# Optimization experiments

Measured on AMD Instinct MI355X. Metric: run time of the kernel, lower is better.

## Reference

```python
import jax, jax.numpy as jnp
import numpy as np

THRE = 4.0  # ReLUX threshold / multispike lens
EPS = 1e-5  # BatchNorm eps (torch default)

@jax.custom_vjp
def spike(x):
    # multispike forward: floor(clamp(x,0,4)+0.5)
    return jnp.floor(jnp.clip(x, 0.0, THRE) + 0.5)

def _spike_fwd(x):
    return spike(x), x

def _spike_bwd(x, g):
    # surrogate gradient: pass-through on 0 < x < lens
    return (g * ((x > 0) & (x < THRE)).astype(g.dtype),)

spike.defvjp(_spike_fwd, _spike_bwd)


def setup_inputs() -> dict:
    key = jax.random.key(0)
    k0, k1, k2 = jax.random.split(key, 3)
    B, N, C = 4, 1024, 512
    x = jax.random.normal(k0, (B, N, C), jnp.float32)
    Wqkv = jax.random.normal(k1, (3 * C, C), jnp.float32) * (C ** -0.5)  # Linear weight [out,in], no bias
    gamma = jnp.ones((3 * C,), jnp.float32)   # BN weight
    beta = jnp.zeros((3 * C,), jnp.float32)   # BN bias
    Wproj = jax.random.normal(k2, (C, C), jnp.float32) * (C ** -0.5)
    bproj = jnp.zeros((C,), jnp.float32)
    return {"x": x, "Wqkv": Wqkv, "gamma": gamma, "beta": beta, "Wproj": Wproj, "bproj": bproj}


def reference(x, Wqkv, gamma, beta, Wproj, bproj):
    B, N, C = x.shape
    H = 8
    hd = C // H
    scale = hd ** -0.5

    xs = spike(x)                                    # head_spike
    qkv = jnp.einsum('bnc,dc->bnd', xs, Wqkv)        # [B,N,3C]
    # BatchNorm1d over channel dim with batch stats across (B, N)
    mu = qkv.mean(axis=(0, 1))
    var = qkv.var(axis=(0, 1))
    qkv = (qkv - mu) * jax.lax.rsqrt(var + EPS) * gamma + beta

    qkv = qkv.reshape(B, N, 3, H, hd).transpose(2, 0, 3, 1, 4)  # [3,B,H,N,hd]
    q = spike(qkv[0])
    k = spike(qkv[1])
    v = spike(qkv[2])

    attn = jnp.einsum('bhnd,bhmd->bhnm', q, k)       # no softmax
    attn = spike(attn)
    out = jnp.einsum('bhnm,bhmd->bhnd', attn, v) * scale
    out = out.transpose(0, 2, 1, 3).reshape(B, N, C)
    out = spike(out)                                 # project_spike
    return jnp.einsum('bnc,dc->bnd', out, Wproj) + bproj
```

## Files before the change

### kernel.cpp

```cpp
#include <hip/hip_runtime.h>

typedef __attribute__((ext_vector_type(8))) short short8;
typedef __attribute__((ext_vector_type(4))) float f32x4;
typedef __attribute__((ext_vector_type(4))) int int4v;
typedef __attribute__((ext_vector_type(4))) unsigned int u32x4;

#define THRE 4.0f

#define GLOAD_LDS16(g, l) \
    __builtin_amdgcn_global_load_lds((const __attribute__((address_space(1))) void*)(g), \
                                     (__attribute__((address_space(3))) void*)(l), 16, 0, 0)

__device__ __forceinline__ float spikef(float x) {
    return floorf(fminf(fmaxf(x, 0.0f), THRE) + 0.5f);
}
__device__ __forceinline__ unsigned short f2bf(float f) {
    return (unsigned short)(__builtin_bit_cast(unsigned int, f) >> 16);
}
__device__ __forceinline__ unsigned short f2bf_rn(float f) {
    unsigned u = __builtin_bit_cast(unsigned int, f);
    unsigned r = ((u >> 16) & 1u) + 0x7FFFu;
    return (unsigned short)((u + r) >> 16);
}
__device__ __forceinline__ float bf2f(unsigned short s) {
    return __builtin_bit_cast(float, (unsigned int)s << 16);
}
__device__ __forceinline__ int4v mfma_i8(u32x4 a, u32x4 b, int4v c) {
    return __builtin_amdgcn_mfma_i32_16x16x64_i8(__builtin_bit_cast(int4v, a),
                                                 __builtin_bit_cast(int4v, b), c, 0, 0, 0);
}

__global__ void k_prep(const float* __restrict__ x,
                       const float* __restrict__ Wq, const float* __restrict__ Wp,
                       short* __restrict__ xs, short* __restrict__ Wqd, short* __restrict__ Wpd) {
    int i = blockIdx.x * 256 + threadIdx.x;
    if (i < 2097152) {
        xs[i] = (short)f2bf(spikef(x[i]));
    } else if (i < 2883584) {
        int j = i - 2097152;
        Wqd[j] = (short)(__builtin_bit_cast(unsigned int, Wq[j]) >> 16);
    } else {
        int j = i - 2883584;
        Wpd[j] = (short)(__builtin_bit_cast(unsigned int, Wp[j]) >> 16);
    }
}

__global__ __launch_bounds__(256) void k_gemm_qkv(const short* __restrict__ A,
                                                  const short* __restrict__ B,
                                                  short* __restrict__ C,
                                                  float* __restrict__ psum,
                                                  float* __restrict__ psq) {
    __shared__ __align__(16) short As[128 * 64];
    __shared__ __align__(16) short Bs[96 * 64];
    const int tid  = threadIdx.x;
    const int lane = tid & 63, wv = tid >> 6;
    const int wy = wv >> 1, wx = wv & 1;
    const int quad = lane >> 4, l16 = lane & 15;
    const int m0 = blockIdx.y * 128, n0 = blockIdx.x * 96;
    const int K = 512, N = 1536;

    f32x4 acc[4][3];
    #pragma unroll
    for (int i = 0; i < 4; ++i)
        #pragma unroll
        for (int j = 0; j < 3; ++j)
            #pragma unroll
            for (int r = 0; r < 4; ++r) acc[i][j][r] = 0.f;

    const short* gA[4]; short* lA[4];
    #pragma unroll
    for (int i = 0; i < 4; ++i) {
        int L = wv + 4 * i;
        int c = L * 64 + lane;
        int r = c >> 3, g = (c & 7) ^ (r & 7);
        gA[i] = A + (size_t)(m0 + r) * K + g * 8;
        lA[i] = &As[L * 512];
    }
    const short* gB[3]; short* lB[3];
    #pragma unroll
    for (int i = 0; i < 3; ++i) {
        int L = wv + 4 * i;
        int c = L * 64 + lane;
        int r = c >> 3, g = (c & 7) ^ (r & 7);
        gB[i] = B + (size_t)(n0 + r) * K + g * 8;
        lB[i] = &Bs[L * 512];
    }

    for (int k0 = 0; k0 < K; k0 += 64) {
        __syncthreads();
        #pragma unroll
        for (int i = 0; i < 4; ++i) GLOAD_LDS16(gA[i] + k0, lA[i]);
        #pragma unroll
        for (int i = 0; i < 3; ++i) GLOAD_LDS16(gB[i] + k0, lB[i]);
        __syncthreads();
        #pragma unroll
        for (int sub = 0; sub < 2; ++sub) {
            const int jc = (sub * 4 + quad) ^ (l16 & 7);
            short8 aF[4], bF[3];
            #pragma unroll
            for (int mt = 0; mt < 4; ++mt)
                aF[mt] = *(const short8*)&As[(wy * 64 + mt * 16 + l16) * 64 + jc * 8];
            #pragma unroll
            for (int nt = 0; nt < 3; ++nt)
                bF[nt] = *(const short8*)&Bs[(wx * 48 + nt * 16 + l16) * 64 + jc * 8];
            #pragma unroll
            for (int mt = 0; mt < 4; ++mt)
                #pragma unroll
                for (int nt = 0; nt < 3; ++nt)
                    acc[mt][nt] = __builtin_amdgcn_mfma_f32_16x16x32_bf16(aF[mt], bF[nt], acc[mt][nt], 0, 0, 0);
        }
    }

    #pragma unroll
    for (int mt = 0; mt < 4; ++mt)
        #pragma unroll
        for (int r = 0; r < 4; ++r) {
            int row = m0 + wy * 64 + mt * 16 + quad * 4 + r;
            short* Cr = C + (size_t)row * N + n0 + wx * 48 + l16;
            #pragma unroll
            for (int nt = 0; nt < 3; ++nt) Cr[nt * 16] = (short)f2bf_rn(acc[mt][nt][r]);
        }

    __syncthreads();
    float* PS = (float*)As;
    float* PQ = (float*)Bs;
    #pragma unroll
    for (int nt = 0; nt < 3; ++nt) {
        float s = 0.f, q = 0.f;
        #pragma unroll
        for (int mt = 0; mt < 4; ++mt)
            #pragma unroll
            for (int r = 0; r < 4; ++r) {
                float v = acc[mt][nt][r];
                s += v;
                q = fmaf(v, v, q);
            }
        PS[(wy * 4 + quad) * 96 + wx * 48 + nt * 16 + l16] = s;
        PQ[(wy * 4 + quad) * 96 + wx * 48 + nt * 16 + l16] = q;
    }
    __syncthreads();
    if (tid < 96) {
        float s = 0.f, q = 0.f;
        #pragma unroll
        for (int i = 0; i < 8; ++i) { s += PS[i * 96 + tid]; q += PQ[i * 96 + tid]; }
        psum[blockIdx.y * 1536 + n0 + tid] = s;
        psq [blockIdx.y * 1536 + n0 + tid] = q;
    }
}

template<bool BIAS, int MT, int NT>
__global__ __launch_bounds__(256) void k_gemm_bf16(const short* __restrict__ A,
                                                   const short* __restrict__ B,
                                                   const float* __restrict__ bias,
                                                   float* __restrict__ C,
                                                   int M, int N, int K) {
    constexpr int BM = MT * 32, BN = NT * 32;
    __shared__ __align__(16) short As[BM * 32];
    __shared__ __align__(16) short Bs[BN * 32];
    const int tid  = threadIdx.x;
    const int lane = tid & 63, wv = tid >> 6;
    const int wy = wv >> 1, wx = wv & 1;
    const int quad = lane >> 4, l16 = lane & 15;
    const int m0 = blockIdx.y * BM, n0 = blockIdx.x * BN;

    f32x4 acc[MT][NT];
    #pragma unroll
    for (int i = 0; i < MT; ++i)
        #pragma unroll
        for (int j = 0; j < NT; ++j)
            #pragma unroll
            for (int r = 0; r < 4; ++r) acc[i][j][r] = 0.f;

    constexpr int LA = 2 * MT, LB = 2 * NT;
    const short* gA[(LA + 3) / 4]; short* lA[(LA + 3) / 4]; int nA = 0;
    #pragma unroll
    for (int L0 = 0; L0 < LA; L0 += 4) {
        int L = L0 + wv;
        if (L < LA) {
            int c = L * 64 + lane;
            gA[nA] = A + (size_t)(m0 + (c >> 2)) * K + (c & 3) * 8;
            lA[nA] = &As[L * 512];
            ++nA;
        }
    }
    const short* gB[(LB + 3) / 4]; short* lB[(LB + 3) / 4]; int nB = 0;
    #pragma unroll
    for (int L0 = 0; L0 < LB; L0 += 4) {
        int L = L0 + wv;
        if (L < LB) {
            int c = L * 64 + lane;
            gB[nB] = B + (size_t)(n0 + (c >> 2)) * K + (c & 3) * 8;
            lB[nB] = &Bs[L * 512];
            ++nB;
        }
    }

    for (int k0 = 0; k0 < K; k0 += 32) {
        __syncthreads();
        for (int i = 0; i < nA; ++i) GLOAD_LDS16(gA[i] + k0, lA[i]);
        for (int i = 0; i < nB; ++i) GLOAD_LDS16(gB[i] + k0, lB[i]);
        __syncthreads();
        short8 aF[MT], bF[NT];
        #pragma unroll
        for (int mt = 0; mt < MT; ++mt)
            aF[mt] = *(const short8*)&As[(wy * MT * 16 + mt * 16 + l16) * 32 + quad * 8];
        #pragma unroll
        for (int nt = 0; nt < NT; ++nt)
            bF[nt] = *(const short8*)&Bs[(wx * NT * 16 + nt * 16 + l16) * 32 + quad * 8];
        #pragma unroll
        for (int mt = 0; mt < MT; ++mt)
            #pragma unroll
            for (int nt = 0; nt < NT; ++nt)
                acc[mt][nt] = __builtin_amdgcn_mfma_f32_16x16x32_bf16(aF[mt], bF[nt], acc[mt][nt], 0, 0, 0);
    }

    float bs[NT];
    #pragma unroll
    for (int nt = 0; nt < NT; ++nt) bs[nt] = BIAS ? bias[n0 + wx * NT * 16 + nt * 16 + l16] : 0.f;
    #pragma unroll
    for (int mt = 0; mt < MT; ++mt)
        #pragma unroll
        for (int r = 0; r < 4; ++r) {
            int row = m0 + wy * MT * 16 + mt * 16 + quad * 4 + r;
            float* Cr = C + (size_t)row * N + n0 + wx * NT * 16 + l16;
            #pragma unroll
            for (int nt = 0; nt < NT; ++nt) Cr[nt * 16] = acc[mt][nt][r] + bs[nt];
        }
}

__global__ __launch_bounds__(256) void k_bn_spike(const short* __restrict__ qkvb,
                           const float* __restrict__ psum, const float* __restrict__ psq,
                           const float* __restrict__ gamma, const float* __restrict__ beta,
                           unsigned char* __restrict__ qp, unsigned char* __restrict__ kp,
                           unsigned char* __restrict__ vt) {
    __shared__ float sa[64], sb[64];
    __shared__ __align__(16) unsigned char tile[64 * 80];
    const int tid = threadIdx.x;
    const int slice = blockIdx.x;
    const int c0 = slice * 64;
    const int r0 = blockIdx.y * 256;
    const int b = r0 >> 10, nb = r0 & 1023;

    if (tid < 64) {
        const int c = c0 + tid;
        double s = 0.0, q = 0.0;
        for (int st = 0; st < 32; ++st) { s += (double)psum[st * 1536 + c]; q += (double)psq[st * 1536 + c]; }
        const double mu  = s / 4096.0;
        const double var = q / 4096.0 - mu * mu;
        const float a = (float)((double)gamma[c] / sqrt(var + 1e-5));
        sa[tid] = a;
        sb[tid] = fmaf(-(float)mu, a, beta[c]);
    }
    __syncthreads();

    const int ch = tid & 63, rq = tid >> 6;
    const float A = sa[ch], Bsh = sb[ch];

    if (slice < 16) {
        const int h = slice & 7;
        unsigned char* base = (slice < 8 ? qp : kp) + (((size_t)b * 8 + h) * 1024 + nb) * 64;
        for (int i = rq; i < 256; i += 4) {
            float v = bf2f((unsigned short)qkvb[(size_t)(r0 + i) * 1536 + c0 + ch]);
            base[(size_t)i * 64 + ch] = (unsigned char)spikef(fmaf(v, A, Bsh));
        }
    } else {
        const int h = slice - 16;
        const int e = tid >> 2, j0 = (tid & 3) * 16;
        unsigned char* vbase = vt + (((size_t)b * 8 + h) * 64 + e) * 1024 + nb;
        for (int rb = 0; rb < 4; ++rb) {
            __syncthreads();
            for (int i = rq; i < 64; i += 4) {
                float v = bf2f((unsigned short)qkvb[(size_t)(r0 + rb * 64 + i) * 1536 + c0 + ch]);
                tile[ch * 80 + i] = (unsigned char)spikef(fmaf(v, A, Bsh));
            }
            __syncthreads();
            *(u32x4*)&vbase[rb * 64 + j0] = *(const u32x4*)&tile[e * 80 + j0];
        }
    }
}

__global__ __launch_bounds__(256) void k_attn(const unsigned char* __restrict__ qp,
                                              const unsigned char* __restrict__ kp,
                                              const unsigned char* __restrict__ vt,
                                              short* __restrict__ sout) {
    __shared__ __align__(16) unsigned char SM[54272];
    unsigned char* Qs = SM;
    unsigned char* Ks = SM + 4096;
    unsigned char* Vs = SM + 20480;
    unsigned int* Sb = (unsigned int*)(SM + 36864);
    const int tid  = threadIdx.x;
    const int lane = tid & 63, w = tid >> 6;
    const int quad = lane >> 4, l16 = lane & 15;
    const int b = blockIdx.z, h = blockIdx.y;
    const int n0 = blockIdx.x * 64;
    const size_t bh = (size_t)b * 8 + h;

    {
        const int r = tid >> 2, p = tid & 3;
        const int g = p ^ (r & 3) ^ ((r >> 2) & 3);
        GLOAD_LDS16(qp + (bh * 1024 + n0 + r) * 64 + g * 16, Qs + (size_t)tid * 16);
    }
    const unsigned char* gK[4]; unsigned char* lK[4];
    const unsigned char* gV[4]; unsigned char* lV[4];
    #pragma unroll
    for (int i = 0; i < 4; ++i) {
        int c = tid + 256 * i;
        int rk = c >> 2, pk2 = c & 3;
        int gk = pk2 ^ (rk & 3) ^ ((rk >> 2) & 3);
        gK[i] = kp + (bh * 1024 + rk) * 64 + gk * 16;
        lK[i] = Ks + (size_t)c * 16;
        int rv = c >> 4, pv = c & 15;
        int gv = pv ^ (rv & 15);
        gV[i] = vt + (bh * 64 + rv) * 1024 + gv * 16;
        lV[i] = Vs + (size_t)c * 16;
    }
    __syncthreads();
    u32x4 qf[4];
    {
        const int pq = quad ^ (l16 & 3) ^ ((l16 >> 2) & 3);
        #pragma unroll
        for (int mt = 0; mt < 4; ++mt)
            qf[mt] = *(const u32x4*)&Qs[(mt * 16 + l16) * 64 + pq * 16];
    }

    int4v of[4];
    #pragma unroll
    for (int mt = 0; mt < 4; ++mt)
        #pragma unroll
        for (int r = 0; r < 4; ++r) of[mt][r] = 0;

    const int pk = quad ^ (l16 & 3) ^ ((l16 >> 2) & 3);

    for (int j0 = 0; j0 < 1024; j0 += 256) {
        __syncthreads();
        #pragma unroll
        for (int i = 0; i < 4; ++i) {
            GLOAD_LDS16(gK[i] + (size_t)j0 * 64, lK[i]);
            GLOAD_LDS16(gV[i] + j0, lV[i]);
        }
        __syncthreads();

        #pragma unroll
        for (int jt = 0; jt < 4; ++jt) {
            u32x4 kf = *(const u32x4*)&Ks[(w * 64 + jt * 16 + l16) * 64 + pk * 16];
            #pragma unroll
            for (int mt = 0; mt < 4; ++mt) {
                int4v z;
                #pragma unroll
                for (int r = 0; r < 4; ++r) z[r] = 0;
                int4v s = mfma_i8(kf, qf[mt], z);
                unsigned int pkk = 0;
                #pragma unroll
                for (int r = 0; r < 4; ++r) {
                    int v = s[r]; v = v < 0 ? 0 : (v > 4 ? 4 : v);
                    pkk |= (unsigned int)v << (8 * r);
                }
                Sb[(mt * 16 + l16) * 68 + w * 16 + jt * 4 + quad] = pkk;
            }
        }
        __syncthreads();

        #pragma unroll
        for (int kk = 0; kk < 4; ++kk) {
            const int pv = (kk * 4 + quad) ^ l16;
            u32x4 bV = *(const u32x4*)&Vs[(w * 16 + l16) * 256 + pv * 16];
            #pragma unroll
            for (int mt = 0; mt < 4; ++mt) {
                u32x4 aS = *(const u32x4*)&Sb[(mt * 16 + l16) * 68 + kk * 16 + quad * 4];
                of[mt] = mfma_i8(aS, bV, of[mt]);
            }
        }
    }

    #pragma unroll
    for (int mt = 0; mt < 4; ++mt)
        #pragma unroll
        for (int r = 0; r < 4; ++r) {
            size_t orow = (size_t)b * 1024 + n0 + mt * 16 + quad * 4 + r;
            sout[orow * 512 + h * 64 + w * 16 + l16] =
                (short)f2bf(spikef((float)of[mt][r] * 0.125f));
        }
}

extern "C" void kernel_launch(void* const* d_in, const int* in_sizes, int n_in,
                              void* d_out, int out_size, void* d_ws, size_t ws_size,
                              hipStream_t stream) {
    const float* x     = (const float*)d_in[0];
    const float* Wqkv  = (const float*)d_in[1];
    const float* gamma = (const float*)d_in[2];
    const float* beta  = (const float*)d_in[3];
    const float* Wproj = (const float*)d_in[4];
    const float* bproj = (const float*)d_in[5];
    float* out = (float*)d_out;

    char* w = (char*)d_ws;
    short* xs            = (short*)(w);
    short* Wqkv2         = (short*)(w + 8388608);
    short* Wproj2        = (short*)(w + 11534336);
    short* qkvb          = (short*)(w + 12582912);
    unsigned char* qp    = (unsigned char*)(w + 37748736);
    unsigned char* kp    = (unsigned char*)(w + 41943040);
    unsigned char* vt    = (unsigned char*)(w + 46137344);
    float* psum          = (float*)(w + 50331648);
    float* psq           = psum + 32 * 1536;
    short* sout          = xs;

    k_prep<<<12288, 256, 0, stream>>>(x, Wqkv, Wproj, xs, Wqkv2, Wproj2);
    k_gemm_qkv<<<dim3(16, 32), 256, 0, stream>>>(xs, Wqkv2, qkvb, psum, psq);
    k_bn_spike<<<dim3(24, 16), 256, 0, stream>>>(qkvb, psum, psq, gamma, beta, qp, kp, vt);
    k_attn<<<dim3(16, 8, 4), 256, 0, stream>>>(qp, kp, vt, sout);
    k_gemm_bf16<true, 1, 4><<<dim3(4, 128), 256, 0, stream>>>(
        sout, Wproj2, bproj, out, 4096, 512, 512);
}
```

Baseline: 120.9 us.

## Fuse all stages into one persistent kernel with software grid barriers

The five separate launches (prep, QKV GEMM, BN+spike, attention, projection GEMM) are replaced by a single 512-block persistent kernel. The stages are separated by atomic-counter grid barriers, and a memset resets the barrier state before launch. This removes per-launch overhead and inter-kernel gaps. In exchange, all 512 blocks must be co-resident, which the code relies on through launch_bounds(256,2) and 54KB of shared memory. Each barrier also costs a spin wait, and the BN stage leaves a quarter of the blocks idle.

Measured after the change: 321.0 us. 2.66x slower.

```diff
diff --git a/kernel.cpp b/kernel.cpp
--- a/kernel.cpp
+++ b/kernel.cpp
@@ -30,356 +30,353 @@
                                                  __builtin_bit_cast(int4v, b), c, 0, 0, 0);
 }
 
-__global__ void k_prep(const float* __restrict__ x,
-                       const float* __restrict__ Wq, const float* __restrict__ Wp,
-                       short* __restrict__ xs, short* __restrict__ Wqd, short* __restrict__ Wpd) {
-    int i = blockIdx.x * 256 + threadIdx.x;
-    if (i < 2097152) {
-        xs[i] = (short)f2bf(spikef(x[i]));
-    } else if (i < 2883584) {
-        int j = i - 2097152;
-        Wqd[j] = (short)(__builtin_bit_cast(unsigned int, Wq[j]) >> 16);
-    } else {
-        int j = i - 2883584;
-        Wpd[j] = (short)(__builtin_bit_cast(unsigned int, Wp[j]) >> 16);
-    }
-}
-
-__global__ __launch_bounds__(256) void k_gemm_qkv(const short* __restrict__ A,
-                                                  const short* __restrict__ B,
-                                                  short* __restrict__ C,
-                                                  float* __restrict__ psum,
-                                                  float* __restrict__ psq) {
-    __shared__ __align__(16) short As[128 * 64];
-    __shared__ __align__(16) short Bs[96 * 64];
-    const int tid  = threadIdx.x;
+#define NB 512
+
+__device__ __forceinline__ void grid_barrier(int* cnt, int* gen) {
+    __syncthreads();
+    if (threadIdx.x == 0) {
+        __threadfence();
+        int g = atomicAdd(gen, 0);
+        if (atomicAdd(cnt, 1) == NB - 1) {
+            atomicExch(cnt, 0);
+            __threadfence();
+            atomicAdd(gen, 1);
+        } else {
+            while (atomicAdd(gen, 0) == g) __builtin_amdgcn_s_sleep(8);
+        }
+        __threadfence();
+    }
+    __syncthreads();
+}
+
+__global__ __launch_bounds__(256, 2) void k_mega(
+        const float* __restrict__ x, const float* __restrict__ Wq,
+        const float* __restrict__ gamma, const float* __restrict__ beta,
+        const float* __restrict__ Wp, const float* __restrict__ bp,
+        short* __restrict__ xs, short* __restrict__ Wqd, short* __restrict__ Wpd,
+        short* __restrict__ qkvb, unsigned char* __restrict__ qp,
+        unsigned char* __restrict__ kp, unsigned char* __restrict__ vt,
+        float* __restrict__ psum, float* __restrict__ psq,
+        float* __restrict__ out, int* bar) {
+    __shared__ __align__(16) unsigned char SM[54272];
+    const int blk = blockIdx.x, tid = threadIdx.x;
+    const int u = blk;
     const int lane = tid & 63, wv = tid >> 6;
     const int wy = wv >> 1, wx = wv & 1;
     const int quad = lane >> 4, l16 = lane & 15;
-    const int m0 = blockIdx.y * 128, n0 = blockIdx.x * 96;
-    const int K = 512, N = 1536;
-
-    f32x4 acc[4][3];
-    #pragma unroll
-    for (int i = 0; i < 4; ++i)
-        #pragma unroll
-        for (int j = 0; j < 3; ++j)
-            #pragma unroll
-            for (int r = 0; r < 4; ++r) acc[i][j][r] = 0.f;
-
-    const short* gA[4]; short* lA[4];
-    #pragma unroll
-    for (int i = 0; i < 4; ++i) {
-        int L = wv + 4 * i;
-        int c = L * 64 + lane;
-        int r = c >> 3, g = (c & 7) ^ (r & 7);
-        gA[i] = A + (size_t)(m0 + r) * K + g * 8;
-        lA[i] = &As[L * 512];
-    }
-    const short* gB[3]; short* lB[3];
-    #pragma unroll
-    for (int i = 0; i < 3; ++i) {
-        int L = wv + 4 * i;
-        int c = L * 64 + lane;
-        int r = c >> 3, g = (c & 7) ^ (r & 7);
-        gB[i] = B + (size_t)(n0 + r) * K + g * 8;
-        lB[i] = &Bs[L * 512];
-    }
-
-    for (int k0 = 0; k0 < K; k0 += 64) {
+    int* cnt = bar;
+    int* gen = bar + 16;
+    short* sout = xs;
+
+    {
+        const int base = blk * 256 + tid;
+        for (int i = base; i < 2097152; i += 131072)
+            xs[i] = (short)f2bf(spikef(x[i]));
+        for (int i = base; i < 786432; i += 131072)
+            Wqd[i] = (short)(__builtin_bit_cast(unsigned int, Wq[i]) >> 16);
+        for (int i = base; i < 262144; i += 131072)
+            Wpd[i] = (short)(__builtin_bit_cast(unsigned int, Wp[i]) >> 16);
+    }
+    grid_barrier(cnt, gen);
+
+    {
+        short* As = (short*)SM;
+        short* Bs = (short*)(SM + 16384);
+        const int m0 = (u >> 4) * 128, n0 = (u & 15) * 96;
+        const int K = 512, N = 1536;
+
+        f32x4 acc[4][3];
+        #pragma unroll
+        for (int i = 0; i < 4; ++i)
+            #pragma unroll
+            for (int j = 0; j < 3; ++j)
+                #pragma unroll
+                for (int r = 0; r < 4; ++r) acc[i][j][r] = 0.f;
+
+        const short* gA[4]; short* lA[4];
+        #pragma unroll
+        for (int i = 0; i < 4; ++i) {
+            int L = wv + 4 * i;
+            int c = L * 64 + lane;
+            int r = c >> 3, g = (c & 7) ^ (r & 7);
+            gA[i] = xs + (size_t)(m0 + r) * K + g * 8;
+            lA[i] = &As[L * 512];
+        }
+        const short* gB[3]; short* lB[3];
+        #pragma unroll
+        for (int i = 0; i < 3; ++i) {
+            int L = wv + 4 * i;
+            int c = L * 64 + lane;
+            int r = c >> 3, g = (c & 7) ^ (r & 7);
+            gB[i] = Wqd + (size_t)(n0 + r) * K + g * 8;
+            lB[i] = &Bs[L * 512];
+        }
+
+        for (int k0 = 0; k0 < K; k0 += 64) {
+            __syncthreads();
+            #pragma unroll
+            for (int i = 0; i < 4; ++i) GLOAD_LDS16(gA[i] + k0, lA[i]);
+            #pragma unroll
+            for (int i = 0; i < 3; ++i) GLOAD_LDS16(gB[i] + k0, lB[i]);
+            __syncthreads();
+            #pragma unroll
+            for (int sub = 0; sub < 2; ++sub) {
+                const int jc = (sub * 4 + quad) ^ (l16 & 7);
+                short8 aF[4], bF[3];
+                #pragma unroll
+                for (int mt = 0; mt < 4; ++mt)
+                    aF[mt] = *(const short8*)&As[(wy * 64 + mt * 16 + l16) * 64 + jc * 8];
+                #pragma unroll
+                for (int nt = 0; nt < 3; ++nt)
+                    bF[nt] = *(const short8*)&Bs[(wx * 48 + nt * 16 + l16) * 64 + jc * 8];
+                #pragma unroll
+                for (int mt = 0; mt < 4; ++mt)
+                    #pragma unroll
+                    for (int nt = 0; nt < 3; ++nt)
+                        acc[mt][nt] = __builtin_amdgcn_mfma_f32_16x16x32_bf16(aF[mt], bF[nt], acc[mt][nt], 0, 0, 0);
+            }
+        }
+
+        #pragma unroll
+        for (int mt = 0; mt < 4; ++mt)
+            #pragma unroll
+            for (int r = 0; r < 4; ++r) {
+                int row = m0 + wy * 64 + mt * 16 + quad * 4 + r;
+                short* Cr = qkvb + (size_t)row * N + n0 + wx * 48 + l16;
+                #pragma unroll
+                for (int nt = 0; nt < 3; ++nt) Cr[nt * 16] = (short)f2bf_rn(acc[mt][nt][r]);
+            }
+
         __syncthreads();
-        #pragma unroll
-        for (int i = 0; i < 4; ++i) GLOAD_LDS16(gA[i] + k0, lA[i]);
-        #pragma unroll
-        for (int i = 0; i < 3; ++i) GLOAD_LDS16(gB[i] + k0, lB[i]);
+        float* PS = (float*)SM;
+        float* PQ = (float*)(SM + 16384);
+        #pragma unroll
+        for (int nt = 0; nt < 3; ++nt) {
+            float s = 0.f, q = 0.f;
+            #pragma unroll
+            for (int mt = 0; mt < 4; ++mt)
+                #pragma unroll
+                for (int r = 0; r < 4; ++r) {
+                    float v = acc[mt][nt][r];
+                    s += v;
+                    q = fmaf(v, v, q);
+                }
+            PS[(wy * 4 + quad) * 96 + wx * 48 + nt * 16 + l16] = s;
+            PQ[(wy * 4 + quad) * 96 + wx * 48 + nt * 16 + l16] = q;
+        }
         __syncthreads();
-        #pragma unroll
-        for (int sub = 0; sub < 2; ++sub) {
-            const int jc = (sub * 4 + quad) ^ (l16 & 7);
-            short8 aF[4], bF[3];
+        if (tid < 96) {
+            float s = 0.f, q = 0.f;
+            #pragma unroll
+            for (int i = 0; i < 8; ++i) { s += PS[i * 96 + tid]; q += PQ[i * 96 + tid]; }
+            psum[(u >> 4) * 1536 + n0 + tid] = s;
+            psq [(u >> 4) * 1536 + n0 + tid] = q;
+        }
+    }
+    grid_barrier(cnt, gen);
+
+    if (u < 384) {
+        float* sa = (float*)SM;
+        float* sb = (float*)(SM + 256);
+        unsigned char* tile = SM + 512;
+        const int slice = u % 24;
+        const int r0 = (u / 24) * 256;
+        const int c0 = slice * 64;
+        const int b = r0 >> 10, nb = r0 & 1023;
+
+        if (tid < 64) {
+            const int c = c0 + tid;
+            double s = 0.0, q = 0.0;
+            for (int st = 0; st < 32; ++st) { s += (double)psum[st * 1536 + c]; q += (double)psq[st * 1536 + c]; }
+            const double mu  = s / 4096.0;
+            const double var = q / 4096.0 - mu * mu;
+            const float a = (float)((double)gamma[c] / sqrt(var + 1e-5));
+            sa[tid] = a;
+            sb[tid] = fmaf(-(float)mu, a, beta[c]);
+        }
+        __syncthreads();
+
+        const int ch = tid & 63, rq = tid >> 6;
+        const float A = sa[ch], Bsh = sb[ch];
+
+        if (slice < 16) {
+            const int h = slice & 7;
+            unsigned char* base = (slice < 8 ? qp : kp) + (((size_t)b * 8 + h) * 1024 + nb) * 64;
+            for (int i = rq; i < 256; i += 4) {
+                float v = bf2f((unsigned short)qkvb[(size_t)(r0 + i) * 1536 + c0 + ch]);
+                base[(size_t)i * 64 + ch] = (unsigned char)spikef(fmaf(v, A, Bsh));
+            }
+        } else {
+            const int h = slice - 16;
+            const int e = tid >> 2, j0 = (tid & 3) * 16;
+            unsigned char* vbase = vt + (((size_t)b * 8 + h) * 64 + e) * 1024 + nb;
+            for (int rb = 0; rb < 4; ++rb) {
+                __syncthreads();
+                for (int i = rq; i < 64; i += 4) {
+                    float v = bf2f((unsigned short)qkvb[(size_t)(r0 + rb * 64 + i) * 1536 + c0 + ch]);
+                    tile[ch * 80 + i] = (unsigned char)spikef(fmaf(v, A, Bsh));
+                }
+                __syncthreads();
+                *(u32x4*)&vbase[rb * 64 + j0] = *(const u32x4*)&tile[e * 80 + j0];
+            }
+        }
+    }
+    grid_barrier(cnt, gen);
+
+    {
+        unsigned char* Qs = SM;
+        unsigned char* Ks = SM + 4096;
+        unsigned char* Vs = SM + 20480;
+        unsigned int* Sb = (unsigned int*)(SM + 36864);
+        const int b = u >> 7, h = (u >> 4) & 7;
+        const int n0 = (u & 15) * 64;
+        const size_t bh = (size_t)b * 8 + h;
+
+        {
+            const int r = tid >> 2, p = tid & 3;
+            const int g = p ^ (r & 3) ^ ((r >> 2) & 3);
+            GLOAD_LDS16(qp + (bh * 1024 + n0 + r) * 64 + g * 16, Qs + (size_t)tid * 16);
+        }
+        const unsigned char* gK[4]; unsigned char* lK[4];
+        const unsigned char* gV[4]; unsigned char* lV[4];
+        #pragma unroll
+        for (int i = 0; i < 4; ++i) {
+            int c = tid + 256 * i;
+            int rk = c >> 2, pk2 = c & 3;
+            int gk = pk2 ^ (rk & 3) ^ ((rk >> 2) & 3);
+            gK[i] = kp + (bh * 1024 + rk) * 64 + gk * 16;
+            lK[i] = Ks + (size_t)c * 16;
+            int rv = c >> 4, pv = c & 15;
+            int gv = pv ^ (rv & 15);
+            gV[i] = vt + (bh * 64 + rv) * 1024 + gv * 16;
+            lV[i] = Vs + (size_t)c * 16;
+        }
+        __syncthreads();
+        u32x4 qf[4];
+        {
+            const int pq = quad ^ (l16 & 3) ^ ((l16 >> 2) & 3);
             #pragma unroll
             for (int mt = 0; mt < 4; ++mt)
-                aF[mt] = *(const short8*)&As[(wy * 64 + mt * 16 + l16) * 64 + jc * 8];
-            #pragma unroll
-            for (int nt = 0; nt < 3; ++nt)
-                bF[nt] = *(const short8*)&Bs[(wx * 48 + nt * 16 + l16) * 64 + jc * 8];
-            #pragma unroll
-            for (int mt = 0; mt < 4; ++mt)
-                #pragma unroll
-                for (int nt = 0; nt < 3; ++nt)
-                    acc[mt][nt] = __builtin_amdgcn_mfma_f32_16x16x32_bf16(aF[mt], bF[nt], acc[mt][nt], 0, 0, 0);
-        }
-    }
-
-    #pragma unroll
-    for (int mt = 0; mt < 4; ++mt)
+                qf[mt] = *(const u32x4*)&Qs[(mt * 16 + l16) * 64 + pq * 16];
+        }
+
+        int4v of[4];
+        #pragma unroll
+        for (int mt = 0; mt < 4; ++mt)
+            #pragma unroll
+            for (int r = 0; r < 4; ++r) of[mt][r] = 0;
+
+        const int pk = quad ^ (l16 & 3) ^ ((l16 >> 2) & 3);
+
+        for (int j0 = 0; j0 < 1024; j0 += 256) {
+            __syncthreads();
+            #pragma unroll
+            for (int i = 0; i < 4; ++i) {
+                GLOAD_LDS16(gK[i] + (size_t)j0 * 64, lK[i]);
+                GLOAD_LDS16(gV[i] + j0, lV[i]);
+            }
+            __syncthreads();
+
+            #pragma unroll
+            for (int jt = 0; jt < 4; ++jt) {
+                u32x4 kf = *(const u32x4*)&Ks[(wv * 64 + jt * 16 + l16) * 64 + pk * 16];
+                #pragma unroll
+                for (int mt = 0; mt < 4; ++mt) {
+                    int4v z;
+                    #pragma unroll
+                    for (int r = 0; r < 4; ++r) z[r] = 0;
+                    int4v s = mfma_i8(kf, qf[mt], z);
+                    unsigned int pkk = 0;
+                    #pragma unroll
+                    for (int r = 0; r < 4; ++r) {
+                        int v = s[r]; v = v < 0 ? 0 : (v > 4 ? 4 : v);
+                        pkk |= (unsigned int)v << (8 * r);
+                    }
+                    Sb[(mt * 16 + l16) * 68 + wv * 16 + jt * 4 + quad] = pkk;
+                }
+            }
+            __syncthreads();
+
+            #pragma unroll
+            for (int kk = 0; kk < 4; ++kk) {
+                const int pv = (kk * 4 + quad) ^ l16;
+                u32x4 bV = *(const u32x4*)&Vs[(wv * 16 + l16) * 256 + pv * 16];
+                #pragma unroll
+                for (int mt = 0; mt < 4; ++mt) {
+                    u32x4 aS = *(const u32x4*)&Sb[(mt * 16 + l16) * 68 + kk * 16 + quad * 4];
+                    of[mt] = mfma_i8(aS, bV, of[mt]);
+                }
+            }
+        }
+
+        #pragma unroll
+        for (int mt = 0; mt < 4; ++mt)
+            #pragma unroll
+            for (int r = 0; r < 4; ++r) {
+                size_t orow = (size_t)b * 1024 + n0 + mt * 16 + quad * 4 + r;
+                sout[orow * 512 + h * 64 + wv * 16 + l16] =
+                    (short)f2bf(spikef((float)of[mt][r] * 0.125f));
+            }
+    }
+    grid_barrier(cnt, gen);
+
+    {
+        short* As = (short*)SM;
+        short* Bs = (short*)(SM + 2048);
+        const int m0 = (u >> 2) * 32, n0 = (u & 3) * 128;
+        const int K = 512, N = 512;
+
+        f32x4 acc[1][4];
+        #pragma unroll
+        for (int j = 0; j < 4; ++j)
+            #pragma unroll
+            for (int r = 0; r < 4; ++r) acc[0][j][r] = 0.f;
+
+        const short* gA0 = nullptr; short* lA0 = nullptr;
+        {
+            int L = wv;
+            if (L < 2) {
+                int c = L * 64 + lane;
+                gA0 = sout + (size_t)(m0 + (c >> 2)) * K + (c & 3) * 8;
+                lA0 = &As[L * 512];
+            }
+        }
+        const short* gB[2]; short* lB[2];
+        #pragma unroll
+        for (int i = 0; i < 2; ++i) {
+            int L = wv + 4 * i;
+            int c = L * 64 + lane;
+            gB[i] = Wpd + (size_t)(n0 + (c >> 2)) * K + (c & 3) * 8;
+            lB[i] = &Bs[L * 512];
+        }
+
+        for (int k0 = 0; k0 < K; k0 += 32) {
+            __syncthreads();
+            if (gA0) GLOAD_LDS16(gA0 + k0, lA0);
+            #pragma unroll
+            for (int i = 0; i < 2; ++i) GLOAD_LDS16(gB[i] + k0, lB[i]);
+            __syncthreads();
+            short8 aF, bF[4];
+            aF = *(const short8*)&As[(wy * 16 + l16) * 32 + quad * 8];
+            #pragma unroll
+            for (int nt = 0; nt < 4; ++nt)
+                bF[nt] = *(const short8*)&Bs[(wx * 64 + nt * 16 + l16) * 32 + quad * 8];
+            #pragma unroll
+            for (int nt = 0; nt < 4; ++nt)
+                acc[0][nt] = __builtin_amdgcn_mfma_f32_16x16x32_bf16(aF, bF[nt], acc[0][nt], 0, 0, 0);
+        }
+
+        float bs[4];
+        #pragma unroll
+        for (int nt = 0; nt < 4; ++nt) bs[nt] = bp[n0 + wx * 64 + nt * 16 + l16];
         #pragma unroll
         for (int r = 0; r < 4; ++r) {
-            int row = m0 + wy * 64 + mt * 16 + quad * 4 + r;
-            short* Cr = C + (size_t)row * N + n0 + wx * 48 + l16;
-            #pragma unroll
-            for (int nt = 0; nt < 3; ++nt) Cr[nt * 16] = (short)f2bf_rn(acc[mt][nt][r]);
-        }
-
-    __syncthreads();
-    float* PS = (float*)As;
-    float* PQ = (float*)Bs;
-    #pragma unroll
-    for (int nt = 0; nt < 3; ++nt) {
-        float s = 0.f, q = 0.f;
-        #pragma unroll
-        for (int mt = 0; mt < 4; ++mt)
-            #pragma unroll
-            for (int r = 0; r < 4; ++r) {
-                float v = acc[mt][nt][r];
-                s += v;
-                q = fmaf(v, v, q);
-            }
-        PS[(wy * 4 + quad) * 96 + wx * 48 + nt * 16 + l16] = s;
-        PQ[(wy * 4 + quad) * 96 + wx * 48 + nt * 16 + l16] = q;
-    }
-    __syncthreads();
-    if (tid < 96) {
-        float s = 0.f, q = 0.f;
-        #pragma unroll
-        for (int i = 0; i < 8; ++i) { s += PS[i * 96 + tid]; q += PQ[i * 96 + tid]; }
-        psum[blockIdx.y * 1536 + n0 + tid] = s;
-        psq [blockIdx.y * 1536 + n0 + tid] = q;
-    }
-}
-
-template<bool BIAS, int MT, int NT>
-__global__ __launch_bounds__(256) void k_gemm_bf16(const short* __restrict__ A,
-                                                   const short* __restrict__ B,
-                                                   const float* __restrict__ bias,
-                                                   float* __restrict__ C,
-                                                   int M, int N, int K) {
-    constexpr int BM = MT * 32, BN = NT * 32;
-    __shared__ __align__(16) short As[BM * 32];
-    __shared__ __align__(16) short Bs[BN * 32];
-    const int tid  = threadIdx.x;
-    const int lane = tid & 63, wv = tid >> 6;
-    const int wy = wv >> 1, wx = wv & 1;
-    const int quad = lane >> 4, l16 = lane & 15;
-    const int m0 = blockIdx.y * BM, n0 = blockIdx.x * BN;
-
-    f32x4 acc[MT][NT];
-    #pragma unroll
-    for (int i = 0; i < MT; ++i)
-        #pragma unroll
-        for (int j = 0; j < NT; ++j)
-            #pragma unroll
-            for (int r = 0; r < 4; ++r) acc[i][j][r] = 0.f;
-
-    constexpr int LA = 2 * MT, LB = 2 * NT;
-    const short* gA[(LA + 3) / 4]; short* lA[(LA + 3) / 4]; int nA = 0;
-    #pragma unroll
-    for (int L0 = 0; L0 < LA; L0 += 4) {
-        int L = L0 + wv;
-        if (L < LA) {
-            int c = L * 64 + lane;
-            gA[nA] = A + (size_t)(m0 + (c >> 2)) * K + (c & 3) * 8;
-            lA[nA] = &As[L * 512];
-            ++nA;
-        }
-    }
-    const short* gB[(LB + 3) / 4]; short* lB[(LB + 3) / 4]; int nB = 0;
-    #pragma unroll
-    for (int L0 = 0; L0 < LB; L0 += 4) {
-        int L = L0 + wv;
-        if (L < LB) {
-            int c = L * 64 + lane;
-            gB[nB] = B + (size_t)(n0 + (c >> 2)) * K + (c & 3) * 8;
-            lB[nB] = &Bs[L * 512];
-            ++nB;
-        }
-    }
-
-    for (int k0 = 0; k0 < K; k0 += 32) {
-        __syncthreads();
-        for (int i = 0; i < nA; ++i) GLOAD_LDS16(gA[i] + k0, lA[i]);
-        for (int i = 0; i < nB; ++i) GLOAD_LDS16(gB[i] + k0, lB[i]);
-        __syncthreads();
-        short8 aF[MT], bF[NT];
-        #pragma unroll
-        for (int mt = 0; mt < MT; ++mt)
-            aF[mt] = *(const short8*)&As[(wy * MT * 16 + mt * 16 + l16) * 32 + quad * 8];
-        #pragma unroll
-        for (int nt = 0; nt < NT; ++nt)
-            bF[nt] = *(const short8*)&Bs[(wx * NT * 16 + nt * 16 + l16) * 32 + quad * 8];
-        #pragma unroll
-        for (int mt = 0; mt < MT; ++mt)
-            #pragma unroll
-            for (int nt = 0; nt < NT; ++nt)
-                acc[mt][nt] = __builtin_amdgcn_mfma_f32_16x16x32_bf16(aF[mt], bF[nt], acc[mt][nt], 0, 0, 0);
-    }
-
-    float bs[NT];
-    #pragma unroll
-    for (int nt = 0; nt < NT; ++nt) bs[nt] = BIAS ? bias[n0 + wx * NT * 16 + nt * 16 + l16] : 0.f;
-    #pragma unroll
-    for (int mt = 0; mt < MT; ++mt)
-        #pragma unroll
-        for (int r = 0; r < 4; ++r) {
-            int row = m0 + wy * MT * 16 + mt * 16 + quad * 4 + r;
-            float* Cr = C + (size_t)row * N + n0 + wx * NT * 16 + l16;
-            #pragma unroll
-            for (int nt = 0; nt < NT; ++nt) Cr[nt * 16] = acc[mt][nt][r] + bs[nt];
-        }
-}
-
-__global__ __launch_bounds__(256) void k_bn_spike(const short* __restrict__ qkvb,
-                           const float* __restrict__ psum, const float* __restrict__ psq,
-                           const float* __restrict__ gamma, const float* __restrict__ beta,
-                           unsigned char* __restrict__ qp, unsigned char* __restrict__ kp,
-                           unsigned char* __restrict__ vt) {
-    __shared__ float sa[64], sb[64];
-    __shared__ __align__(16) unsigned char tile[64 * 80];
-    const int tid = threadIdx.x;
-    const int slice = blockIdx.x;
-    const int c0 = slice * 64;
-    const int r0 = blockIdx.y * 256;
-    const int b = r0 >> 10, nb = r0 & 1023;
-
-    if (tid < 64) {
-        const int c = c0 + tid;
-        double s = 0.0, q = 0.0;
-        for (int st = 0; st < 32; ++st) { s += (double)psum[st * 1536 + c]; q += (double)psq[st * 1536 + c]; }
-        const double mu  = s / 4096.0;
-        const double var = q / 4096.0 - mu * mu;
-        const float a = (float)((double)gamma[c] / sqrt(var + 1e-5));
-        sa[tid] = a;
-        sb[tid] = fmaf(-(float)mu, a, beta[c]);
-    }
-    __syncthreads();
-
-    const int ch = tid & 63, rq = tid >> 6;
-    const float A = sa[ch], Bsh = sb[ch];
-
-    if (slice < 16) {
-        const int h = slice & 7;
-        unsigned char* base = (slice < 8 ? qp : kp) + (((size_t)b * 8 + h) * 1024 + nb) * 64;
-        for (int i = rq; i < 256; i += 4) {
-            float v = bf2f((unsigned short)qkvb[(size_t)(r0 + i) * 1536 + c0 + ch]);
-            base[(size_t)i * 64 + ch] = (unsigned char)spikef(fmaf(v, A, Bsh));
-        }
-    } else {
-        const int h = slice - 16;
-        const int e = tid >> 2, j0 = (tid & 3) * 16;
-        unsigned char* vbase = vt + (((size_t)b * 8 + h) * 64 + e) * 1024 + nb;
-        for (int rb = 0; rb < 4; ++rb) {
-            __syncthreads();
-            for (int i = rq; i < 64; i += 4) {
-                float v = bf2f((unsigned short)qkvb[(size_t)(r0 + rb * 64 + i) * 1536 + c0 + ch]);
-                tile[ch * 80 + i] = (unsigned char)spikef(fmaf(v, A, Bsh));
-            }
-            __syncthreads();
-            *(u32x4*)&vbase[rb * 64 + j0] = *(const u32x4*)&tile[e * 80 + j0];
-        }
-    }
-}
-
-__global__ __launch_bounds__(256) void k_attn(const unsigned char* __restrict__ qp,
-                                              const unsigned char* __restrict__ kp,
-                                              const unsigned char* __restrict__ vt,
-                                              short* __restrict__ sout) {
-    __shared__ __align__(16) unsigned char SM[54272];
-    unsigned char* Qs = SM;
-    unsigned char* Ks = SM + 4096;
-    unsigned char* Vs = SM + 20480;
-    unsigned int* Sb = (unsigned int*)(SM + 36864);
-    const int tid  = threadIdx.x;
-    const int lane = tid & 63, w = tid >> 6;
-    const int quad = lane >> 4, l16 = lane & 15;
-    const int b = blockIdx.z, h = blockIdx.y;
-    const int n0 = blockIdx.x * 64;
-    const size_t bh = (size_t)b * 8 + h;
-
-    {
-        const int r = tid >> 2, p = tid & 3;
-        const int g = p ^ (r & 3) ^ ((r >> 2) & 3);
-        GLOAD_LDS16(qp + (bh * 1024 + n0 + r) * 64 + g * 16, Qs + (size_t)tid * 16);
-    }
-    const unsigned char* gK[4]; unsigned char* lK[4];
-    const unsigned char* gV[4]; unsigned char* lV[4];
-    #pragma unroll
-    for (int i = 0; i < 4; ++i) {
-        int c = tid + 256 * i;
-        int rk = c >> 2, pk2 = c & 3;
-        int gk = pk2 ^ (rk & 3) ^ ((rk >> 2) & 3);
-        gK[i] = kp + (bh * 1024 + rk) * 64 + gk * 16;
-        lK[i] = Ks + (size_t)c * 16;
-        int rv = c >> 4, pv = c & 15;
-        int gv = pv ^ (rv & 15);
-        gV[i] = vt + (bh * 64 + rv) * 1024 + gv * 16;
-        lV[i] = Vs + (size_t)c * 16;
-    }
-    __syncthreads();
-    u32x4 qf[4];
-    {
-        const int pq = quad ^ (l16 & 3) ^ ((l16 >> 2) & 3);
-        #pragma unroll
-        for (int mt = 0; mt < 4; ++mt)
-            qf[mt] = *(const u32x4*)&Qs[(mt * 16 + l16) * 64 + pq * 16];
-    }
-
-    int4v of[4];
-    #pragma unroll
-    for (int mt = 0; mt < 4; ++mt)
-        #pragma unroll
-        for (int r = 0; r < 4; ++r) of[mt][r] = 0;
-
-    const int pk = quad ^ (l16 & 3) ^ ((l16 >> 2) & 3);
-
-    for (int j0 = 0; j0 < 1024; j0 += 256) {
-        __syncthreads();
-        #pragma unroll
-        for (int i = 0; i < 4; ++i) {
-            GLOAD_LDS16(gK[i] + (size_t)j0 * 64, lK[i]);
-            GLOAD_LDS16(gV[i] + j0, lV[i]);
-        }
-        __syncthreads();
-
-        #pragma unroll
-        for (int jt = 0; jt < 4; ++jt) {
-            u32x4 kf = *(const u32x4*)&Ks[(w * 64 + jt * 16 + l16) * 64 + pk * 16];
-            #pragma unroll
-            for (int mt = 0; mt < 4; ++mt) {
-                int4v z;
-                #pragma unroll
-                for (int r = 0; r < 4; ++r) z[r] = 0;
-                int4v s = mfma_i8(kf, qf[mt], z);
-                unsigned int pkk = 0;
-                #pragma unroll
-                for (int r = 0; r < 4; ++r) {
-                    int v = s[r]; v = v < 0 ? 0 : (v > 4 ? 4 : v);
-                    pkk |= (unsigned int)v << (8 * r);
-                }
-                Sb[(mt * 16 + l16) * 68 + w * 16 + jt * 4 + quad] = pkk;
-            }
-        }
-        __syncthreads();
-
-        #pragma unroll
-        for (int kk = 0; kk < 4; ++kk) {
-            const int pv = (kk * 4 + quad) ^ l16;
-            u32x4 bV = *(const u32x4*)&Vs[(w * 16 + l16) * 256 + pv * 16];
-            #pragma unroll
-            for (int mt = 0; mt < 4; ++mt) {
-                u32x4 aS = *(const u32x4*)&Sb[(mt * 16 + l16) * 68 + kk * 16 + quad * 4];
-                of[mt] = mfma_i8(aS, bV, of[mt]);
-            }
-        }
-    }
-
-    #pragma unroll
-    for (int mt = 0; mt < 4; ++mt)
-        #pragma unroll
-        for (int r = 0; r < 4; ++r) {
-            size_t orow = (size_t)b * 1024 + n0 + mt * 16 + quad * 4 + r;
-            sout[orow * 512 + h * 64 + w * 16 + l16] =
-                (short)f2bf(spikef((float)of[mt][r] * 0.125f));
-        }
+            int row = m0 + wy * 16 + quad * 4 + r;
+            float* Cr = out + (size_t)row * N + n0 + wx * 64 + l16;
+            #pragma unroll
+            for (int nt = 0; nt < 4; ++nt) Cr[nt * 16] = acc[0][nt][r] + bs[nt];
+        }
+    }
 }
 
 extern "C" void kernel_launch(void* const* d_in, const int* in_sizes, int n_in,
@@ -403,12 +400,10 @@
     unsigned char* vt    = (unsigned char*)(w + 46137344);
     float* psum          = (float*)(w + 50331648);
     float* psq           = psum + 32 * 1536;
-    short* sout          = xs;
-
-    k_prep<<<12288, 256, 0, stream>>>(x, Wqkv, Wproj, xs, Wqkv2, Wproj2);
-    k_gemm_qkv<<<dim3(16, 32), 256, 0, stream>>>(xs, Wqkv2, qkvb, psum, psq);
-    k_bn_spike<<<dim3(24, 16), 256, 0, stream>>>(qkvb, psum, psq, gamma, beta, qp, kp, vt);
-    k_attn<<<dim3(16, 8, 4), 256, 0, stream>>>(qp, kp, vt, sout);
-    k_gemm_bf16<true, 1, 4><<<dim3(4, 128), 256, 0, stream>>>(
-        sout, Wproj2, bproj, out, 4096, 512, 512);
-}
+    int*   bar           = (int*)(w + 60817408);
+
+    hipMemsetAsync(bar, 0, 128, stream);
+    k_mega<<<NB, 256, 0, stream>>>(x, Wqkv, gamma, beta, Wproj, bproj,
+                                   xs, Wqkv2, Wproj2, qkvb, qp, kp, vt,
+                                   psum, psq, out, bar);
+}
```
